# Optimization experiments

Hardware: AMD Instinct MI355X
Metric: run time of the kernel (lower is better)

Reference implementation:

```python
import jax, jax.numpy as jnp
import numpy as np

B, T, C = 8, 2048, 1024
H, D = 16, 64
DLOW = 64  # D_DECAY = D_AAA = D_MV = D_GATE = 64
EPS_LN = 1e-5


def setup_inputs() -> dict:
    key = jax.random.key(0)
    ks = jax.random.split(key, 26)
    p = lambda k, shape, s=0.02: (jax.random.normal(k, shape, jnp.float32) * s)
    u = lambda k, shape: jax.random.uniform(k, shape, jnp.float32)
    return {
        "x":   jax.random.normal(ks[0], (B, T, C), jnp.float32),
        # token-shift mix coefficients (1,1,C)
        "x_r": u(ks[1], (1, 1, C)), "x_w": u(ks[2], (1, 1, C)),
        "x_k": u(ks[3], (1, 1, C)), "x_v": u(ks[4], (1, 1, C)),
        "x_a": u(ks[5], (1, 1, C)), "x_g": u(ks[6], (1, 1, C)),
        # decay lora: w1 [C,DLOW], w2 [DLOW,H], w0 [1,1,H,1]
        "w0": p(ks[7], (1, 1, H, 1)), "w1": p(ks[8], (C, DLOW)), "w2": p(ks[9], (DLOW, H)),
        # in-context lr lora
        "a0": p(ks[10], (1, 1, H, 1)), "a1": p(ks[11], (C, DLOW)), "a2": p(ks[12], (DLOW, H)),
        # value residual lora
        "v0": p(ks[13], (1, 1, C)), "v1": p(ks[14], (C, DLOW)), "v2": p(ks[15], (DLOW, C)),
        # gate lora
        "g1": p(ks[16], (C, DLOW)), "g2": p(ks[17], (DLOW, C)),
        "k_k": 0.85 + p(ks[18], (1, 1, C)),
        "r_k": p(ks[19], (H, D)),
        # main projections, stored [in, out] so x @ W matches nn.Linear
        "Wr": p(ks[20], (C, C)), "Wk": p(ks[21], (C, C)),
        "Wv": p(ks[22], (C, C)), "Wo": p(ks[23], (C, C)),
        # GroupNorm(n_head, n_embd) affine params
        "ln_w": jnp.ones((C,), jnp.float32) + p(ks[24], (C,)),
        "ln_b": p(ks[25], (C,)),
    }


def reference(x, x_r, x_w, x_k, x_v, x_a, x_g,
              w0, w1, w2, a0, a1, a2, v0, v1, v2, g1, g2,
              k_k, r_k, Wr, Wk, Wv, Wo, ln_w, ln_b):
    Bb, Tt, Cc = x.shape
    Hh, Dd = r_k.shape
    # token shift: sx = x_t - x_{t-1} (zero-padded)
    xx = jnp.concatenate([jnp.zeros((Bb, 1, Cc), x.dtype), x[:, :-1]], axis=1)
    sx = x - xx
    xr = x + sx * x_r
    xw = x + sx * x_w
    xk = x + sx * x_k
    xv = x + sx * x_v
    xa = x + sx * x_a
    xg = x + sx * x_g

    r = (xr @ Wr).reshape(Bb, Tt, Hh, Dd)
    # decay in (0, exp(-0.5)): exp(-softplus(-(w0 + lora)) - 0.5)
    w = jnp.exp(-jax.nn.softplus(-(w0 + (jnp.tanh(xw @ w1) @ w2).reshape(Bb, Tt, Hh, 1))) - 0.5)
    k = xk @ Wk
    v = xv @ Wv
    v_res_gate = jax.nn.sigmoid(v0 + jnp.tanh(xv @ v1) @ v2)
    v = v + (v - v) * v_res_gate  # no-op, kept for faithfulness
    a = jax.nn.sigmoid(a0 + (jnp.tanh(xa @ a1) @ a2).reshape(Bb, Tt, Hh, 1))
    g = jax.nn.sigmoid(jnp.tanh(xg @ g1) @ g2)

    kk = (k * k_k).reshape(Bb, Tt, Hh, Dd)
    kk = kk / jnp.maximum(jnp.linalg.norm(kk, axis=-1, keepdims=True), 1e-12)
    vh = v.reshape(Bb, Tt, Hh, Dd)

    # WKV linear recurrence: state = state * w_t + kk_t * v_t * a_t
    kv = (kk * vh * a).astype(jnp.float32)            # [B,T,H,D]
    w_t = jnp.moveaxis(w.astype(jnp.float32), 1, 0)   # [T,B,H,1]
    kv_t = jnp.moveaxis(kv, 1, 0)                     # [T,B,H,D]

    def step(state, inputs):
        wt, kvt = inputs
        state = state * wt + kvt
        return state, state

    init = jnp.zeros((Bb, Hh, Dd), jnp.float32)
    _, states = jax.lax.scan(step, init, (w_t, kv_t))  # [T,B,H,D]
    x_wkv = jnp.moveaxis(states, 0, 1).astype(x.dtype)  # [B,T,H,D]

    x_wkv = x_wkv * r
    bonus = jnp.sum(r * kk * r_k, axis=-1, keepdims=True) * vh
    x_wkv = x_wkv + bonus  # [B,T,H,D]

    # GroupNorm(H groups over C channels), per (B*T) sample
    mean = x_wkv.mean(axis=-1, keepdims=True)
    var = x_wkv.var(axis=-1, keepdims=True)
    xn = (x_wkv - mean) * jax.lax.rsqrt(var + EPS_LN)
    xn = xn.reshape(Bb, Tt, Cc) * ln_w + ln_b

    return (xn * g) @ Wo
```

## Files before the change

kernel.cpp:

```cpp
#include <hip/hip_runtime.h>


typedef __bf16 bf16;
typedef __attribute__((ext_vector_type(8))) __bf16 bf16x8;
typedef __attribute__((ext_vector_type(4))) float f32x4;

#define TBTOK 16384
#define TSEQ  2048
#define CDIM  1024
#define HN    16
#define CHUNK 32
#define NCH   64

__device__ __forceinline__ float wredsum(float v) {
#pragma unroll
  for (int o = 32; o > 0; o >>= 1) v += __shfl_xor(v, o, 64);
  return v;
}
__device__ __forceinline__ float redsum8(float v) {
#pragma unroll
  for (int o = 4; o > 0; o >>= 1) v += __shfl_xor(v, o, 64);
  return v;
}
__device__ __forceinline__ float sigmf(float x) { return 1.f / (1.f + expf(-x)); }

__device__ __forceinline__ void gl_lds16(const bf16* g, bf16* l) {
  __builtin_amdgcn_global_load_lds(
      (const __attribute__((address_space(1))) unsigned int*)g,
      (__attribute__((address_space(3))) unsigned int*)l, 16, 0, 0);
}

__global__ __launch_bounds__(256) void prep_kern(
    const float* __restrict__ x, const float* __restrict__ mr,
    const float* __restrict__ mk, const float* __restrict__ mv,
    bf16* __restrict__ xr, bf16* __restrict__ xk, bf16* __restrict__ xv,
    bf16* __restrict__ xbf,
    const float* __restrict__ Wr, const float* __restrict__ Wk,
    const float* __restrict__ Wv, const float* __restrict__ Wo,
    const float* __restrict__ w1, const float* __restrict__ a1, const float* __restrict__ g1,
    const float* __restrict__ mw, const float* __restrict__ ma, const float* __restrict__ mg,
    const float* __restrict__ g2, const float* __restrict__ w2, const float* __restrict__ a2,
    bf16* __restrict__ WrT, bf16* __restrict__ WkT, bf16* __restrict__ WvT, bf16* __restrict__ WoT,
    bf16* __restrict__ Bcat, bf16* __restrict__ g2T,
    bf16* __restrict__ w2T, bf16* __restrict__ a2T, float* __restrict__ zpad) {
  int bid0 = blockIdx.x;
  int tid = threadIdx.x;
  if (bid0 < 8192) {
    long i8 = ((long)bid0 * 256 + tid) * 8;
    int m = (int)(i8 >> 10);
    int c = (int)(i8 & 1023);
    f32x4 x0 = *(const f32x4*)(x + i8);
    f32x4 x1 = *(const f32x4*)(x + i8 + 4);
    f32x4 p0 = {0.f, 0.f, 0.f, 0.f}, p1 = {0.f, 0.f, 0.f, 0.f};
    if ((m & (TSEQ - 1)) != 0) {
      p0 = *(const f32x4*)(x + i8 - CDIM);
      p1 = *(const f32x4*)(x + i8 - CDIM + 4);
    }
    f32x4 r0 = *(const f32x4*)(mr + c), r1 = *(const f32x4*)(mr + c + 4);
    f32x4 k0 = *(const f32x4*)(mk + c), k1 = *(const f32x4*)(mk + c + 4);
    f32x4 v0 = *(const f32x4*)(mv + c), v1 = *(const f32x4*)(mv + c + 4);
    bf16x8 or_, ok_, ov_, ox_;
#pragma unroll
    for (int j = 0; j < 4; j++) {
      float s0 = x0[j] - p0[j], s1 = x1[j] - p1[j];
      or_[j] = (bf16)(x0[j] + s0 * r0[j]); or_[4 + j] = (bf16)(x1[j] + s1 * r1[j]);
      ok_[j] = (bf16)(x0[j] + s0 * k0[j]); ok_[4 + j] = (bf16)(x1[j] + s1 * k1[j]);
      ov_[j] = (bf16)(x0[j] + s0 * v0[j]); ov_[4 + j] = (bf16)(x1[j] + s1 * v1[j]);
      ox_[j] = (bf16)x0[j];                ox_[4 + j] = (bf16)x1[j];
    }
    *(bf16x8*)(xr + i8) = or_;
    *(bf16x8*)(xk + i8) = ok_;
    *(bf16x8*)(xv + i8) = ov_;
    *(bf16x8*)(xbf + i8) = ox_;
    return;
  }
  int bid = bid0 - 8192;
  int tx = tid & 31, ty = tid >> 5;
  __shared__ bf16 tile[32][33];
  if (bid < 4096) {
    int sel = bid >> 10, t = bid & 1023;
    int k0 = (t >> 5) * 32, n0 = (t & 31) * 32;
    const float* src = sel == 0 ? Wr : (sel == 1 ? Wk : (sel == 2 ? Wv : Wo));
    bf16* dst = sel == 0 ? WrT : (sel == 1 ? WkT : (sel == 2 ? WvT : WoT));
#pragma unroll
    for (int i = 0; i < 4; i++)
      tile[ty + i * 8][tx] = (bf16)src[(long)(k0 + ty + i * 8) * 1024 + n0 + tx];
    __syncthreads();
#pragma unroll
    for (int i = 0; i < 4; i++)
      dst[(long)(n0 + ty + i * 8) * 1024 + k0 + tx] = tile[tx][ty + i * 8];
  } else if (bid < 4480) {
    int idx = bid - 4096;
    int mat = idx >> 7, rem = idx & 127;
    int half = rem >> 6, t = rem & 63;
    int k0 = (t >> 1) * 32, n0 = (t & 1) * 32;
    const float* W = mat == 0 ? w1 : (mat == 1 ? a1 : g1);
    const float* mx = mat == 0 ? mw : (mat == 1 ? ma : mg);
#pragma unroll
    for (int i = 0; i < 4; i++) {
      int k = k0 + ty + i * 8;
      float s = half == 0 ? (1.f + mx[k]) : (-mx[k]);
      tile[ty + i * 8][tx] = (bf16)(s * W[(long)k * 64 + n0 + tx]);
    }
    __syncthreads();
#pragma unroll
    for (int i = 0; i < 4; i++)
      Bcat[(long)(mat * 64 + n0 + ty + i * 8) * 2048 + half * 1024 + k0 + tx] =
          tile[tx][ty + i * 8];
  } else if (bid < 4544) {
    int t = bid - 4480;
    int k0 = (t >> 5) * 32, n0 = (t & 31) * 32;
#pragma unroll
    for (int i = 0; i < 4; i++)
      tile[ty + i * 8][tx] = (bf16)g2[(long)(k0 + ty + i * 8) * 1024 + n0 + tx];
    __syncthreads();
#pragma unroll
    for (int i = 0; i < 4; i++)
      g2T[(long)(n0 + ty + i * 8) * 64 + k0 + tx] = tile[tx][ty + i * 8];
  } else {
#pragma unroll
    for (int rep = 0; rep < 4; rep++) {
      int idx = rep * 256 + tid;
      int k = idx >> 4, h = idx & 15;
      w2T[h * 64 + k] = (bf16)w2[idx];
      a2T[h * 64 + k] = (bf16)a2[idx];
    }
    if (tid < 64) zpad[tid] = 0.f;
  }
}

template <typename OT>
__global__ __launch_bounds__(512, 2) void gemm256_kern(
    const bf16* __restrict__ A0, const bf16* __restrict__ A1, const bf16* __restrict__ A2,
    const bf16* __restrict__ BT0, const bf16* __restrict__ BT1, const bf16* __restrict__ BT2,
    OT* __restrict__ out0, OT* __restrict__ out1, OT* __restrict__ out2,
    int K, int nbpm) {
  int nwg = gridDim.x;
  int id = blockIdx.x;
  int qq = nwg >> 3;
  int wg = (id & 7) * qq + (id >> 3);
  int mat = wg / nbpm;
  int rem = wg - mat * nbpm;
  int m0 = (rem & 63) << 8;
  int n0 = (rem >> 6) << 8;
  const bf16* Am = mat == 0 ? A0 : (mat == 1 ? A1 : A2);
  const bf16* BTm = mat == 0 ? BT0 : (mat == 1 ? BT1 : BT2);
  OT* out = mat == 0 ? out0 : (mat == 1 ? out1 : out2);

  __shared__ bf16 Al[2][256 * 64];
  __shared__ bf16 Bl[2][256 * 64];

  int tid = threadIdx.x;
  int w = tid >> 6, lane = tid & 63, quad = lane >> 4, lr = lane & 15;
  int wr = w >> 2, wc = w & 3;

  int r0 = tid >> 3, slot = tid & 7;
  int kg = (slot ^ (r0 & 7)) * 8;
  const bf16* ag = Am + (long)(m0 + r0) * K + kg;
  const bf16* bg = BTm + (long)(n0 + r0) * K + kg;
  long rstep = (long)64 * K;
  bf16* laW = &Al[0][0] + w * 512;
  bf16* lbW = &Bl[0][0] + w * 512;

  auto stage = [&](int bsel, int t) {
    const bf16* a = ag + t * 64;
    const bf16* b = bg + t * 64;
    bf16* la = laW + bsel * 16384;
    bf16* lb = lbW + bsel * 16384;
#pragma unroll
    for (int s = 0; s < 4; s++) gl_lds16(a + s * rstep, la + s * 4096);
#pragma unroll
    for (int s = 0; s < 4; s++) gl_lds16(b + s * rstep, lb + s * 4096);
  };

  f32x4 acc[8][4] = {};
  stage(0, 0);
  stage(1, 1);
  asm volatile("s_waitcnt vmcnt(8)" ::: "memory");
  __builtin_amdgcn_s_barrier();

  int NT = K >> 6;
#pragma unroll 1
  for (int t = 0; t < NT; t++) {
    int cur = t & 1;
    const bf16* Ab = &Al[0][0] + cur * 16384;
    const bf16* Bb = &Bl[0][0] + cur * 16384;
    bf16x8 af[4][2], bfr[4][2];
#pragma unroll
    for (int j = 0; j < 4; j++) {
      int rb = wc * 64 + j * 16 + lr;
#pragma unroll
      for (int ks = 0; ks < 2; ks++)
        bfr[j][ks] = *(const bf16x8*)&Bb[rb * 64 + (((ks * 4 + quad) ^ (rb & 7)) * 8)];
    }
#pragma unroll
    for (int i = 0; i < 4; i++) {
      int ra = wr * 128 + i * 16 + lr;
#pragma unroll
      for (int ks = 0; ks < 2; ks++)
        af[i][ks] = *(const bf16x8*)&Ab[ra * 64 + (((ks * 4 + quad) ^ (ra & 7)) * 8)];
    }
    __builtin_amdgcn_s_barrier();
    asm volatile("s_waitcnt lgkmcnt(0)" ::: "memory");
    __builtin_amdgcn_sched_barrier(0);
    __builtin_amdgcn_s_setprio(1);
#pragma unroll
    for (int ks = 0; ks < 2; ks++)
#pragma unroll
      for (int i = 0; i < 4; i++)
#pragma unroll
        for (int j = 0; j < 4; j++)
          acc[i][j] =
              __builtin_amdgcn_mfma_f32_16x16x32_bf16(af[i][ks], bfr[j][ks], acc[i][j], 0, 0, 0);
    __builtin_amdgcn_s_setprio(0);
    __builtin_amdgcn_s_barrier();
#pragma unroll
    for (int i = 0; i < 4; i++) {
      int ra = wr * 128 + 64 + i * 16 + lr;
#pragma unroll
      for (int ks = 0; ks < 2; ks++)
        af[i][ks] = *(const bf16x8*)&Ab[ra * 64 + (((ks * 4 + quad) ^ (ra & 7)) * 8)];
    }
    __builtin_amdgcn_s_barrier();
    asm volatile("s_waitcnt lgkmcnt(0)" ::: "memory");
    __builtin_amdgcn_sched_barrier(0);
    __builtin_amdgcn_s_setprio(1);
#pragma unroll
    for (int ks = 0; ks < 2; ks++)
#pragma unroll
      for (int i = 0; i < 4; i++)
#pragma unroll
        for (int j = 0; j < 4; j++)
          acc[4 + i][j] = __builtin_amdgcn_mfma_f32_16x16x32_bf16(af[i][ks], bfr[j][ks],
                                                                  acc[4 + i][j], 0, 0, 0);
    __builtin_amdgcn_s_setprio(0);
    __builtin_amdgcn_s_barrier();
    if (t + 2 < NT) {
      stage(cur, t + 2);
      asm volatile("s_waitcnt vmcnt(8)" ::: "memory");
    } else {
      asm volatile("s_waitcnt vmcnt(0)" ::: "memory");
    }
    __builtin_amdgcn_s_barrier();
  }

#pragma unroll
  for (int i = 0; i < 8; i++)
#pragma unroll
    for (int j = 0; j < 4; j++)
#pragma unroll
      for (int rg = 0; rg < 4; rg++) {
        int row = m0 + wr * 128 + i * 16 + quad * 4 + rg;
        int col = n0 + wc * 64 + j * 16 + lr;
        out[(long)row * CDIM + col] = (OT)acc[i][j][rg];
      }
}

__global__ __launch_bounds__(256) void stage1_kern(
    const bf16* __restrict__ xbf, const bf16* __restrict__ Bcat,
    const float* __restrict__ zpad, const bf16* __restrict__ w2T, const bf16* __restrict__ a2T,
    const float* __restrict__ w0, const float* __restrict__ a0,
    bf16* __restrict__ t1g, float* __restrict__ w_arr, float* __restrict__ a_arr) {
  int m0 = blockIdx.x * 64;
  int part = blockIdx.y;
  __shared__ bf16 Al[64 * 32];
  __shared__ bf16 Bl[128 * 32];
  __shared__ bf16 Lt1[64 * 136];

  int tid = threadIdx.x;
  int w = tid >> 6, lane = tid & 63, quad = lane >> 4, lr = lane & 15;
  int wm = w * 16;

  int r0 = tid >> 2, kc0 = (tid & 3) * 8;
  int m = m0 + r0;
  const bf16* asrc = xbf + (long)m * CDIM + kc0;
  bool firstrow = (m & (TSEQ - 1)) == 0;
  const bf16* psrc = firstrow ? (const bf16*)zpad : xbf + (long)(m - 1) * CDIM + kc0;
  int pstep = firstrow ? 0 : 32;
  int brow0 = part ? 128 : 0;
  const bf16* bs0 = Bcat + (long)(brow0 + r0) * 2048 + kc0;
  const bf16* bs1 = bs0 + (long)64 * 2048;
  bf16* la = Al + w * 512;
  bf16* lb0 = Bl + w * 512;
  bf16* lb1 = Bl + 2048 + w * 512;

  if (part == 0) {
    f32x4 acc[8] = {};
#pragma unroll 1
    for (int kk = 0; kk < 64; kk++) {
      if (kk < 32) { gl_lds16(asrc, la); asrc += 32; }
      else         { gl_lds16(psrc, la); psrc += pstep; }
      gl_lds16(bs0, lb0);
      gl_lds16(bs1, lb1);
      bs0 += 32; bs1 += 32;
      __syncthreads();
      bf16x8 af = *(const bf16x8*)&Al[(wm + lr) * 32 + quad * 8];
#pragma unroll
      for (int nf = 0; nf < 8; nf++) {
        bf16x8 bff = *(const bf16x8*)&Bl[(nf * 16 + lr) * 32 + quad * 8];
        acc[nf] = __builtin_amdgcn_mfma_f32_16x16x32_bf16(af, bff, acc[nf], 0, 0, 0);
      }
      __syncthreads();
    }
#pragma unroll
    for (int nf = 0; nf < 8; nf++)
#pragma unroll
      for (int rg = 0; rg < 4; rg++) {
        int row = wm + quad * 4 + rg;
        Lt1[row * 136 + nf * 16 + lr] = (bf16)tanhf(acc[nf][rg]);
      }
    __syncthreads();
#pragma unroll
    for (int rep = 0; rep < 4; rep++) {
      int idx = rep * 256 + tid;
      int row = idx >> 4, h = idx & 15;
      const bf16* rw = &Lt1[row * 136];
      const bf16* ra = rw + 64;
      const bf16* ww = w2T + h * 64;
      const bf16* aw = a2T + h * 64;
      float dw = 0.f, da = 0.f;
#pragma unroll
      for (int k = 0; k < 64; k++) {
        dw += (float)rw[k] * (float)ww[k];
        da += (float)ra[k] * (float)aw[k];
      }
      w_arr[h * TBTOK + m0 + row] = 0.60653066f * sigmf(w0[h] + dw);
      a_arr[h * TBTOK + m0 + row] = sigmf(a0[h] + da);
    }
  } else {
    f32x4 acc[4] = {};
#pragma unroll 1
    for (int kk = 0; kk < 64; kk++) {
      if (kk < 32) { gl_lds16(asrc, la); asrc += 32; }
      else         { gl_lds16(psrc, la); psrc += pstep; }
      gl_lds16(bs0, lb0);
      bs0 += 32;
      __syncthreads();
      bf16x8 af = *(const bf16x8*)&Al[(wm + lr) * 32 + quad * 8];
#pragma unroll
      for (int nf = 0; nf < 4; nf++) {
        bf16x8 bff = *(const bf16x8*)&Bl[(nf * 16 + lr) * 32 + quad * 8];
        acc[nf] = __builtin_amdgcn_mfma_f32_16x16x32_bf16(af, bff, acc[nf], 0, 0, 0);
      }
      __syncthreads();
    }
#pragma unroll
    for (int nf = 0; nf < 4; nf++)
#pragma unroll
      for (int rg = 0; rg < 4; rg++) {
        int row = wm + quad * 4 + rg;
        t1g[(long)(m0 + row) * 64 + nf * 16 + lr] = (bf16)tanhf(acc[nf][rg]);
      }
  }
}

__global__ __launch_bounds__(256) void scan1_kern(
    const bf16* __restrict__ k_buf, const bf16* __restrict__ v_buf, const bf16* __restrict__ r_buf,
    const float* __restrict__ k_k, const float* __restrict__ r_k,
    const float* __restrict__ a_arr, const float* __restrict__ w_arr,
    float* __restrict__ kv2, float* __restrict__ Parr, float* __restrict__ bonus,
    float* __restrict__ Lend) {
  int wid = blockIdx.x * 4 + (threadIdx.x >> 6);
  int lane = threadIdx.x & 63;
  int bh = wid >> 6, c = wid & 63;
  int b = bh >> 4, h = bh & 15;
  int mstart = b * TSEQ + c * CHUNK;
  int kc = h * 64 + lane;
  float kkc = k_k[kc], rkc = r_k[kc];
  float st = 0.f, cw = 1.f;
  long mbase = (long)mstart * CDIM + kc;
  int hm = h * TBTOK + mstart;
  long sbase = ((long)hm) * 64 + lane;
  float kf = (float)k_buf[mbase] * kkc;
  float vf = (float)v_buf[mbase];
  float rf = (float)r_buf[mbase];
  float af = a_arr[hm];
  float wt = w_arr[hm];
  for (int t = 0; t < CHUNK; t++) {
    float kf_n = 0.f, vf_n = 0.f, rf_n = 0.f, af_n = 0.f, wt_n = 0.f;
    if (t < CHUNK - 1) {
      kf_n = (float)k_buf[mbase + CDIM] * kkc;
      vf_n = (float)v_buf[mbase + CDIM];
      rf_n = (float)r_buf[mbase + CDIM];
      af_n = a_arr[hm + 1];
      wt_n = w_arr[hm + 1];
    }
    float ss = wredsum(kf * kf);
    float kkn = kf / fmaxf(sqrtf(ss), 1e-12f);
    st = st * wt + kkn * vf * af;
    kv2[sbase] = st;
    cw *= wt;
    float bs = wredsum(rf * kkn * rkc);
    if (lane == 0) {
      Parr[hm] = cw;
      bonus[(mstart + t) * HN + h] = bs;
    }
    kf = kf_n; vf = vf_n; rf = rf_n; af = af_n; wt = wt_n;
    mbase += CDIM; hm += 1; sbase += 64;
  }
  Lend[(long)wid * 64 + lane] = st;
}

__global__ __launch_bounds__(256) void gate_post_kern(
    const bf16* __restrict__ t1g, const bf16* __restrict__ g2T,
    const float* __restrict__ kv2, const float* __restrict__ Parr,
    const float* __restrict__ Lend, const float* __restrict__ bonus,
    bf16* __restrict__ r_buf, const bf16* __restrict__ v_buf,
    const float* __restrict__ ln_w, const float* __restrict__ ln_b) {
  int ncol0 = blockIdx.x * 128;
  int m0 = blockIdx.y * 128;

  __shared__ bf16 Al[128 * 32];
  __shared__ bf16 Bl[128 * 32];
  __shared__ bf16 gtile[128 * 136];

  int tid = threadIdx.x;
  int w = tid >> 6, lane = tid & 63, quad = lane >> 4, lr = lane & 15;
  int wm = (w & 1) * 64, wn = (w >> 1) * 64;

  f32x4 acc[4][4] = {};

  int r0 = tid >> 2, kc0 = (tid & 3) * 8;
  const bf16* ag0 = t1g + (long)(m0 + r0) * 64 + kc0;
  const bf16* ag1 = ag0 + (long)64 * 64;
  const bf16* bg0 = g2T + (long)(ncol0 + r0) * 64 + kc0;
  const bf16* bg1 = bg0 + (long)64 * 64;
  bf16* la0 = Al + w * 512;
  bf16* la1 = Al + 2048 + w * 512;
  bf16* lb0 = Bl + w * 512;
  bf16* lb1 = Bl + 2048 + w * 512;

  for (int k0 = 0; k0 < 64; k0 += 32) {
    gl_lds16(ag0, la0);
    gl_lds16(ag1, la1);
    gl_lds16(bg0, lb0);
    gl_lds16(bg1, lb1);
    ag0 += 32; ag1 += 32; bg0 += 32; bg1 += 32;
    __syncthreads();
    bf16x8 af[4], bff[4];
#pragma unroll
    for (int i = 0; i < 4; i++) af[i] = *(const bf16x8*)&Al[(wm + i * 16 + lr) * 32 + quad * 8];
#pragma unroll
    for (int j = 0; j < 4; j++) bff[j] = *(const bf16x8*)&Bl[(wn + j * 16 + lr) * 32 + quad * 8];
#pragma unroll
    for (int i = 0; i < 4; i++)
#pragma unroll
      for (int j = 0; j < 4; j++)
        acc[i][j] = __builtin_amdgcn_mfma_f32_16x16x32_bf16(af[i], bff[j], acc[i][j], 0, 0, 0);
    __syncthreads();
  }
#pragma unroll
  for (int i = 0; i < 4; i++)
#pragma unroll
    for (int j = 0; j < 4; j++)
#pragma unroll
      for (int rg = 0; rg < 4; rg++) {
        int row = wm + i * 16 + quad * 4 + rg;
        int col = wn + j * 16 + lr;
        gtile[row * 136 + col] = (bf16)sigmf(acc[i][j][rg]);
      }
  __syncthreads();

  int c_loc = (tid & 15) * 8;
  int col_g = ncol0 + c_loc;
  int h = col_g >> 6;
  int d0 = col_g & 63;
  f32x4 lnw0 = *(const f32x4*)(ln_w + col_g);
  f32x4 lnw1 = *(const f32x4*)(ln_w + col_g + 4);
  f32x4 lnb0 = *(const f32x4*)(ln_b + col_g);
  f32x4 lnb1 = *(const f32x4*)(ln_b + col_g + 4);
#pragma unroll
  for (int jj = 0; jj < 8; jj++) {
    int row = jj * 16 + (tid >> 4);
    int row_g = m0 + row;
    int b = row_g >> 11;
    int ch = (row_g & (TSEQ - 1)) >> 5;
    long kvb = ((long)h * TBTOK + row_g) * 64 + d0;
    f32x4 st0 = *(const f32x4*)(kv2 + kvb);
    f32x4 st1 = *(const f32x4*)(kv2 + kvb + 4);
    f32x4 cy0 = {0.f, 0.f, 0.f, 0.f}, cy1 = {0.f, 0.f, 0.f, 0.f};
    if (ch != 0) {
      long lb = ((long)((b * 16 + h) * NCH + ch - 1)) * 64 + d0;
      cy0 = *(const f32x4*)(Lend + lb);
      cy1 = *(const f32x4*)(Lend + lb + 4);
    }
    float pw = Parr[h * TBTOK + row_g];
    float bs = bonus[row_g * HN + h];
    long rb = (long)row_g * CDIM + col_g;
    bf16x8 rf8 = *(const bf16x8*)(r_buf + rb);
    bf16x8 vf8 = *(const bf16x8*)(v_buf + rb);
    bf16x8 g8 = *(const bf16x8*)&gtile[row * 136 + c_loc];
    float xw[8];
#pragma unroll
    for (int q = 0; q < 4; q++) {
      xw[q]     = (st0[q] + pw * cy0[q]) * (float)rf8[q]     + bs * (float)vf8[q];
      xw[4 + q] = (st1[q] + pw * cy1[q]) * (float)rf8[4 + q] + bs * (float)vf8[4 + q];
    }
    float sum = 0.f;
#pragma unroll
    for (int q = 0; q < 8; q++) sum += xw[q];
    float mn = redsum8(sum) * (1.f / 64.f);
    float vs = 0.f;
#pragma unroll
    for (int q = 0; q < 8; q++) {
      xw[q] -= mn;
      vs += xw[q] * xw[q];
    }
    float var = redsum8(vs) * (1.f / 64.f);
    float rq = rsqrtf(var + 1e-5f);
    bf16x8 o8;
#pragma unroll
    for (int q = 0; q < 4; q++) {
      o8[q]     = (bf16)((xw[q] * rq * lnw0[q] + lnb0[q]) * (float)g8[q]);
      o8[4 + q] = (bf16)((xw[4 + q] * rq * lnw1[q] + lnb1[q]) * (float)g8[4 + q]);
    }
    *(bf16x8*)(r_buf + rb) = o8;
  }
}

extern "C" void kernel_launch(void* const* d_in, const int* in_sizes, int n_in,
                              void* d_out, int out_size, void* d_ws, size_t ws_size,
                              hipStream_t stream) {
  const float* x    = (const float*)d_in[0];
  const float* x_r  = (const float*)d_in[1];
  const float* x_w  = (const float*)d_in[2];
  const float* x_k  = (const float*)d_in[3];
  const float* x_v  = (const float*)d_in[4];
  const float* x_a  = (const float*)d_in[5];
  const float* x_g  = (const float*)d_in[6];
  const float* w0   = (const float*)d_in[7];
  const float* w1   = (const float*)d_in[8];
  const float* w2   = (const float*)d_in[9];
  const float* a0   = (const float*)d_in[10];
  const float* a1   = (const float*)d_in[11];
  const float* a2   = (const float*)d_in[12];
  const float* g1   = (const float*)d_in[16];
  const float* g2   = (const float*)d_in[17];
  const float* k_k  = (const float*)d_in[18];
  const float* r_k  = (const float*)d_in[19];
  const float* Wr   = (const float*)d_in[20];
  const float* Wk   = (const float*)d_in[21];
  const float* Wv   = (const float*)d_in[22];
  const float* Wo   = (const float*)d_in[23];
  const float* ln_w = (const float*)d_in[24];
  const float* ln_b = (const float*)d_in[25];
  float* out = (float*)d_out;

  char* p = (char*)d_ws;
  auto carve = [&](size_t bytes) {
    void* r = (void*)p;
    p += (bytes + 255) & ~(size_t)255;
    return r;
  };
  bf16* WrT = (bf16*)carve(1024 * 1024 * 2);
  bf16* WkT = (bf16*)carve(1024 * 1024 * 2);
  bf16* WvT = (bf16*)carve(1024 * 1024 * 2);
  bf16* WoT = (bf16*)carve(1024 * 1024 * 2);
  bf16* Bcat = (bf16*)carve(192 * 2048 * 2);
  bf16* g2T  = (bf16*)carve(1024 * 64 * 2);
  bf16* w2T  = (bf16*)carve(16 * 64 * 2);
  bf16* a2T  = (bf16*)carve(16 * 64 * 2);
  float* zpad = (float*)carve(64 * 4);
  bf16* t1g   = (bf16*)carve((size_t)TBTOK * 64 * 2);
  bf16* r_buf = (bf16*)carve((size_t)TBTOK * CDIM * 2);
  bf16* k_buf = (bf16*)carve((size_t)TBTOK * CDIM * 2);
  bf16* v_buf = (bf16*)carve((size_t)TBTOK * CDIM * 2);
  float* w_arr = (float*)carve((size_t)TBTOK * HN * 4);
  float* a_arr = (float*)carve((size_t)TBTOK * HN * 4);
  float* bonus = (float*)carve((size_t)TBTOK * HN * 4);
  float* Parr  = (float*)carve((size_t)TBTOK * HN * 4);
  float* Lend  = (float*)carve((size_t)128 * NCH * 64 * 4);
  bf16* xr  = (bf16*)carve((size_t)TBTOK * CDIM * 2);
  bf16* xk  = (bf16*)carve((size_t)TBTOK * CDIM * 2);
  bf16* xv  = (bf16*)carve((size_t)TBTOK * CDIM * 2);
  bf16* xbf = (bf16*)carve((size_t)TBTOK * CDIM * 2);
  float* kv2 = (float*)xv;

  prep_kern<<<dim3(8192 + 4545), 256, 0, stream>>>(
      x, x_r, x_k, x_v, xr, xk, xv, xbf,
      Wr, Wk, Wv, Wo, w1, a1, g1, x_w, x_a, x_g, g2, w2, a2,
      WrT, WkT, WvT, WoT, Bcat, g2T, w2T, a2T, zpad);
  stage1_kern<<<dim3(TBTOK / 64, 2), 256, 0, stream>>>(
      xbf, Bcat, zpad, w2T, a2T, w0, a0, t1g, w_arr, a_arr);
  gemm256_kern<bf16><<<dim3(768), 512, 0, stream>>>(
      xr, xk, xv, WrT, WkT, WvT, r_buf, k_buf, v_buf, 1024, 256);
  scan1_kern<<<dim3(128 * NCH / 4), 256, 0, stream>>>(
      k_buf, v_buf, r_buf, k_k, r_k, a_arr, w_arr, kv2, Parr, bonus, Lend);
  gate_post_kern<<<dim3(8, TBTOK / 128), 256, 0, stream>>>(
      t1g, g2T, kv2, Parr, Lend, bonus, r_buf, v_buf, ln_w, ln_b);
  gemm256_kern<float><<<dim3(256), 512, 0, stream>>>(
      r_buf, r_buf, r_buf, WoT, WoT, WoT, out, out, out, 1024, 256);
}
```

Before: 548.5 us.

## Split GEMM LDS buffers into half-tiles and interleave loads with quarter MFMA phases

Restructures the 256x256 bf16 GEMM main loop so each K-step is split into four quadrant MFMA phases, and LDS buffers are split into 128-row halves. Global-to-LDS loads for the next K-steps are issued per half-tile between the MFMA phases rather than as one block at the end of the step. The intent is finer-grained overlap of memory traffic with compute and earlier reuse of freed buffer halves. The trade-off is many more barriers per iteration and a more fragile wait-count schedule. The unrolled loop handles two K-steps per iteration and assumes an even tile count.

```diff
diff --git a/kernel.cpp b/kernel.cpp
--- a/kernel.cpp
+++ b/kernel.cpp
@@ -129,6 +129,43 @@
   }
 }
 
+#define BARRIER __builtin_amdgcn_s_barrier()
+#define LGKM0                                              \
+  do {                                                     \
+    asm volatile("s_waitcnt lgkmcnt(0)" ::: "memory");     \
+    __builtin_amdgcn_sched_barrier(0);                     \
+  } while (0)
+
+#define READ_A(HALFP, QM)                                                                \
+  {                                                                                      \
+    const bf16* _h = (HALFP);                                                            \
+    _Pragma("unroll") for (int i = 0; i < 4; i++) {                                      \
+      int ra = (QM)*64 + i * 16 + lr;                                                    \
+      _Pragma("unroll") for (int ks = 0; ks < 2; ks++)                                   \
+          af[i][ks] = *(const bf16x8*)&_h[ra * 64 + (((ks * 4 + quad) ^ (ra & 7)) * 8)]; \
+    }                                                                                    \
+  }
+
+#define READ_B(HALFP, QN)                                                                \
+  {                                                                                      \
+    const bf16* _h = (HALFP);                                                            \
+    _Pragma("unroll") for (int jj = 0; jj < 2; jj++) {                                   \
+      int rb = bro + ((QN)*2 + jj) * 16 + lr;                                            \
+      _Pragma("unroll") for (int ks = 0; ks < 2; ks++)                                   \
+          bfr[(QN)*2 + jj][ks] =                                                         \
+              *(const bf16x8*)&_h[rb * 64 + (((ks * 4 + quad) ^ (rb & 7)) * 8)];         \
+    }                                                                                    \
+  }
+
+#define MFMA16(QM, QN)                                                            \
+  __builtin_amdgcn_s_setprio(1);                                                  \
+  _Pragma("unroll") for (int ks = 0; ks < 2; ks++)                                \
+  _Pragma("unroll") for (int i = 0; i < 4; i++)                                   \
+  _Pragma("unroll") for (int jj = 0; jj < 2; jj++)                                \
+      acc[(QM)*4 + i][(QN)*2 + jj] = __builtin_amdgcn_mfma_f32_16x16x32_bf16(     \
+          af[i][ks], bfr[(QN)*2 + jj][ks], acc[(QM)*4 + i][(QN)*2 + jj], 0, 0, 0);\
+  __builtin_amdgcn_s_setprio(0);
+
 template <typename OT>
 __global__ __launch_bounds__(512, 2) void gemm256_kern(
     const bf16* __restrict__ A0, const bf16* __restrict__ A1, const bf16* __restrict__ A2,
@@ -147,101 +184,97 @@
   const bf16* BTm = mat == 0 ? BT0 : (mat == 1 ? BT1 : BT2);
   OT* out = mat == 0 ? out0 : (mat == 1 ? out1 : out2);
 
-  __shared__ bf16 Al[2][256 * 64];
-  __shared__ bf16 Bl[2][256 * 64];
+  __shared__ bf16 Al[2][2][128 * 64];
+  __shared__ bf16 Bl[2][2][128 * 64];
 
   int tid = threadIdx.x;
   int w = tid >> 6, lane = tid & 63, quad = lane >> 4, lr = lane & 15;
   int wr = w >> 2, wc = w & 3;
-
-  int r0 = tid >> 3, slot = tid & 7;
-  int kg = (slot ^ (r0 & 7)) * 8;
-  const bf16* ag = Am + (long)(m0 + r0) * K + kg;
-  const bf16* bg = BTm + (long)(n0 + r0) * K + kg;
-  long rstep = (long)64 * K;
-  bf16* laW = &Al[0][0] + w * 512;
-  bf16* lbW = &Bl[0][0] + w * 512;
-
-  auto stage = [&](int bsel, int t) {
-    const bf16* a = ag + t * 64;
-    const bf16* b = bg + t * 64;
-    bf16* la = laW + bsel * 16384;
-    bf16* lb = lbW + bsel * 16384;
-#pragma unroll
-    for (int s = 0; s < 4; s++) gl_lds16(a + s * rstep, la + s * 4096);
-#pragma unroll
-    for (int s = 0; s < 4; s++) gl_lds16(b + s * rstep, lb + s * 4096);
+  int hb = wc >> 1, bro = (wc & 1) * 64;
+
+  int swz = ((tid & 7) ^ ((tid >> 3) & 7)) * 8;
+  const bf16* aBase = Am + (long)(m0 + (tid >> 3)) * K + swz;
+  const bf16* bBase = BTm + (long)(n0 + (tid >> 3)) * K + swz;
+
+  auto stgA = [&](int db, int h, int t) {
+    const bf16* g = aBase + (long)(h * 128) * K + t * 64;
+    bf16* l = &Al[db][h][0] + w * 512;
+    gl_lds16(g, l);
+    gl_lds16(g + (long)64 * K, l + 4096);
   };
+  auto stgB = [&](int db, int h, int t) {
+    const bf16* g = bBase + (long)(h * 128) * K + t * 64;
+    bf16* l = &Bl[db][h][0] + w * 512;
+    gl_lds16(g, l);
+    gl_lds16(g + (long)64 * K, l + 4096);
+  };
+
+  const bf16* A0p = &Al[0][wr][0];
+  const bf16* A1p = &Al[1][wr][0];
+  const bf16* B0p = &Bl[0][hb][0];
+  const bf16* B1p = &Bl[1][hb][0];
 
   f32x4 acc[8][4] = {};
-  stage(0, 0);
-  stage(1, 1);
-  asm volatile("s_waitcnt vmcnt(8)" ::: "memory");
-  __builtin_amdgcn_s_barrier();
-
-  int NT = K >> 6;
+  bf16x8 af[4][2], bfr[4][2];
+
+  int NT = K >> 6, NU = NT >> 1;
+
+  stgB(0, 0, 0); stgA(0, 0, 0); stgA(0, 1, 0); stgB(0, 1, 0);
+  stgB(1, 0, 1); stgA(1, 0, 1);
+  asm volatile("s_waitcnt vmcnt(4)" ::: "memory");
+  BARRIER;
+
 #pragma unroll 1
-  for (int t = 0; t < NT; t++) {
-    int cur = t & 1;
-    const bf16* Ab = &Al[0][0] + cur * 16384;
-    const bf16* Bb = &Bl[0][0] + cur * 16384;
-    bf16x8 af[4][2], bfr[4][2];
-#pragma unroll
-    for (int j = 0; j < 4; j++) {
-      int rb = wc * 64 + j * 16 + lr;
-#pragma unroll
-      for (int ks = 0; ks < 2; ks++)
-        bfr[j][ks] = *(const bf16x8*)&Bb[rb * 64 + (((ks * 4 + quad) ^ (rb & 7)) * 8)];
-    }
-#pragma unroll
-    for (int i = 0; i < 4; i++) {
-      int ra = wr * 128 + i * 16 + lr;
-#pragma unroll
-      for (int ks = 0; ks < 2; ks++)
-        af[i][ks] = *(const bf16x8*)&Ab[ra * 64 + (((ks * 4 + quad) ^ (ra & 7)) * 8)];
-    }
-    __builtin_amdgcn_s_barrier();
-    asm volatile("s_waitcnt lgkmcnt(0)" ::: "memory");
+  for (int u = 0; u < NU; u++) {
+    int t1 = 2 * u + 1, t2 = 2 * u + 2, t3 = 2 * u + 3;
+    READ_A(A0p, 0);
+    READ_B(B0p, 0);
+    stgA(1, 1, t1);
+    asm volatile("s_waitcnt lgkmcnt(8)" ::: "memory");
+    BARRIER; LGKM0;
+    MFMA16(0, 0);
+    BARRIER;
+    READ_B(B0p, 1);
+    stgB(1, 1, t1);
+    BARRIER; LGKM0;
+    MFMA16(0, 1);
+    BARRIER;
+    READ_A(A0p, 1);
+    if (t2 < NT) stgB(0, 0, t2);
+    BARRIER; LGKM0;
+    MFMA16(1, 1);
+    BARRIER;
+    if (t2 < NT) stgA(0, 0, t2);
+    BARRIER;
     __builtin_amdgcn_sched_barrier(0);
-    __builtin_amdgcn_s_setprio(1);
-#pragma unroll
-    for (int ks = 0; ks < 2; ks++)
-#pragma unroll
-      for (int i = 0; i < 4; i++)
-#pragma unroll
-        for (int j = 0; j < 4; j++)
-          acc[i][j] =
-              __builtin_amdgcn_mfma_f32_16x16x32_bf16(af[i][ks], bfr[j][ks], acc[i][j], 0, 0, 0);
-    __builtin_amdgcn_s_setprio(0);
-    __builtin_amdgcn_s_barrier();
-#pragma unroll
-    for (int i = 0; i < 4; i++) {
-      int ra = wr * 128 + 64 + i * 16 + lr;
-#pragma unroll
-      for (int ks = 0; ks < 2; ks++)
-        af[i][ks] = *(const bf16x8*)&Ab[ra * 64 + (((ks * 4 + quad) ^ (ra & 7)) * 8)];
-    }
-    __builtin_amdgcn_s_barrier();
-    asm volatile("s_waitcnt lgkmcnt(0)" ::: "memory");
+    MFMA16(1, 0);
+    if (t2 < NT) { asm volatile("s_waitcnt vmcnt(4)" ::: "memory"); }
+    else         { asm volatile("s_waitcnt vmcnt(0)" ::: "memory"); }
+    BARRIER;
+    READ_A(A1p, 0);
+    READ_B(B1p, 0);
+    if (t2 < NT) stgA(0, 1, t2);
+    asm volatile("s_waitcnt lgkmcnt(8)" ::: "memory");
+    BARRIER; LGKM0;
+    MFMA16(0, 0);
+    BARRIER;
+    READ_B(B1p, 1);
+    if (t2 < NT) stgB(0, 1, t2);
+    BARRIER; LGKM0;
+    MFMA16(0, 1);
+    BARRIER;
+    READ_A(A1p, 1);
+    if (t3 < NT) stgB(1, 0, t3);
+    BARRIER; LGKM0;
+    MFMA16(1, 1);
+    BARRIER;
+    if (t3 < NT) stgA(1, 0, t3);
+    BARRIER;
     __builtin_amdgcn_sched_barrier(0);
-    __builtin_amdgcn_s_setprio(1);
-#pragma unroll
-    for (int ks = 0; ks < 2; ks++)
-#pragma unroll
-      for (int i = 0; i < 4; i++)
-#pragma unroll
-        for (int j = 0; j < 4; j++)
-          acc[4 + i][j] = __builtin_amdgcn_mfma_f32_16x16x32_bf16(af[i][ks], bfr[j][ks],
-                                                                  acc[4 + i][j], 0, 0, 0);
-    __builtin_amdgcn_s_setprio(0);
-    __builtin_amdgcn_s_barrier();
-    if (t + 2 < NT) {
-      stage(cur, t + 2);
-      asm volatile("s_waitcnt vmcnt(8)" ::: "memory");
-    } else {
-      asm volatile("s_waitcnt vmcnt(0)" ::: "memory");
-    }
-    __builtin_amdgcn_s_barrier();
+    MFMA16(1, 0);
+    if (t3 < NT) { asm volatile("s_waitcnt vmcnt(4)" ::: "memory"); }
+    else         { asm volatile("s_waitcnt vmcnt(0)" ::: "memory"); }
+    BARRIER;
   }
 
 #pragma unroll
```

New measurement: 553.3 us. Within noise of the previous version (+0.9%).
